# Kernel optimization log

Measured on AMD Instinct MI355X. Metric: run time of the kernel, lower is better.

## Reference

```python
import jax, jax.numpy as jnp
import numpy as np

LN_EPS = 1e-5

def _linear(x, W, b):
    # torch nn.Linear equivalent with W stored as [in, out]
    return jnp.einsum('bsd,de->bse', x, W) + b

def setup_inputs() -> dict:
    key = jax.random.key(0)
    ks = jax.random.split(key, 8)
    B, S, D = 4, 4096, 1024
    scale = 0.02
    inp = {
        'x': jax.random.normal(ks[0], (B, S, D), dtype=jnp.float32),
        'Wk': jax.random.normal(ks[1], (D, D), dtype=jnp.float32) * scale,
        'bk': jnp.zeros((D,), jnp.float32),
        'Wv': jax.random.normal(ks[2], (D, D), dtype=jnp.float32) * scale,
        'bv': jnp.zeros((D,), jnp.float32),
        'Wq': jax.random.normal(ks[3], (D, D), dtype=jnp.float32) * scale,
        'bq': jnp.zeros((D,), jnp.float32),
        'Wkp': jax.random.normal(ks[4], (D, D), dtype=jnp.float32) * scale,
        'bkp': jnp.zeros((D,), jnp.float32),
        'Wqp': jax.random.normal(ks[5], (D, D), dtype=jnp.float32) * scale,
        'bqp': jnp.zeros((D,), jnp.float32),
        'ln_g': jnp.ones((D,), jnp.float32),
        'ln_b': jnp.zeros((D,), jnp.float32),
        'Wo': jax.random.normal(ks[6], (D, D), dtype=jnp.float32) * scale,
        'bo': jnp.zeros((D,), jnp.float32),
        'idx': jax.random.permutation(ks[7], S)[:32].astype(jnp.int32),
        'chunk_size': 64,
    }
    return inp

def _ortho_loss(kc, ks_, idx):
    # sample rows, pairwise Re(conj(z_i) z_j) = cos_i cos_j + sin_i sin_j
    B, _, D = kc.shape
    n = idx.shape[0]
    cs = kc[:, idx, :]                                # [B, n, D]
    sn = ks_[:, idx, :]
    dot = cs[:, :, None, :] * cs[:, None, :, :] + sn[:, :, None, :] * sn[:, None, :, :]  # [B,n,n,D]
    mask = (~jnp.eye(n, dtype=bool))[None, :, :, None].astype(dot.dtype)
    denom = jnp.float32(n * (n - 1)) * D + 1e-6       # mask.sum() * dim + eps
    return jnp.sum(dot * dot * mask) / denom

def reference(x, Wk, bk, Wv, bv, Wq, bq, Wkp, bkp, Wqp, bqp, ln_g, ln_b, Wo, bo, idx, chunk_size):
    B, S, D = x.shape
    key = _linear(x, Wk, bk)
    value = _linear(x, Wv, bv)
    query = _linear(x, Wq, bq)
    key_phase = _linear(key, Wkp, bkp)
    query_phase = _linear(query, Wqp, bqp)
    kc, ksin = jnp.cos(key_phase), jnp.sin(key_phase)
    qc, qsin = jnp.cos(query_phase), jnp.sin(query_phase)
    ortho = _ortho_loss(kc, ksin, idx)
    br = value * kc
    bi = value * ksin
    pad = (-S) % chunk_size
    if pad > 0:
        pw = ((0, 0), (0, pad), (0, 0))
        br = jnp.pad(br, pw); bi = jnp.pad(bi, pw)
        qc = jnp.pad(qc, pw); qsin = jnp.pad(qsin, pw)
    P = S + pad
    nc = P // chunk_size
    shp = (B, nc, chunk_size, D)
    mem_r = jnp.cumsum(br.reshape(shp), axis=2)
    mem_i = jnp.cumsum(bi.reshape(shp), axis=2)
    retrieved = mem_r * qc.reshape(shp) + mem_i * qsin.reshape(shp)
    retrieved = retrieved.reshape(B, P, D)[:, :S]
    retrieved = retrieved / jnp.sqrt(jnp.float32(S))
    mu = jnp.mean(retrieved, axis=-1, keepdims=True)
    var = jnp.var(retrieved, axis=-1, keepdims=True)
    ln = (retrieved - mu) * jax.lax.rsqrt(var + LN_EPS) * ln_g + ln_b
    out = x + _linear(ln, Wo, bo)
    return out, ortho
```

## Files before the change

### kernel.cpp

```cpp
#include <hip/hip_runtime.h>
#include <math.h>

#define D_DIM 1024
#define S_DIM 4096
#define B_DIM 4
#define CHUNK 64
#define NC (S_DIM / CHUNK)
#define M_DIM (B_DIM * S_DIM)
#define MD ((size_t)M_DIM * D_DIM)

typedef __bf16 bf16_t;
typedef __attribute__((ext_vector_type(8))) __bf16 bf16x8;
typedef __attribute__((ext_vector_type(4))) __bf16 bf16x4;
typedef __attribute__((ext_vector_type(2))) __bf16 bf16x2;
typedef __attribute__((ext_vector_type(4))) float f32x4;

__device__ __forceinline__ void async_copy16(const void* g, void* lds) {
  __builtin_amdgcn_global_load_lds(
      (const __attribute__((address_space(1))) unsigned int*)g,
      (__attribute__((address_space(3))) unsigned int*)lds, 16, 0, 0);
}

#define SB __builtin_amdgcn_s_barrier()
#define PRIO1 __builtin_amdgcn_s_setprio(1)
#define PRIO0 __builtin_amdgcn_s_setprio(0)

template <int MODE>
__global__ __launch_bounds__(512, 2) void gemm256(const bf16_t* __restrict__ A,
                                                  const bf16_t* __restrict__ Bt,
                                                  const float* __restrict__ bias,
                                                  const float* __restrict__ res,
                                                  float* __restrict__ Cf,
                                                  bf16_t* __restrict__ Cb) {
  constexpr int K = D_DIM;
  constexpr int NB_N = (MODE == 0) ? 12 : 4;
  __shared__ bf16_t sm[65536];

  const int bid = blockIdx.x;
  const int xcd = bid & 7;
  const int slot = bid >> 3;
  const int bm = (xcd * 8 + slot / NB_N) * 256;
  const int bn = (slot % NB_N) * 256;

  const int tid = threadIdx.x;
  const int lane = tid & 63;
  const int wave = tid >> 6;
  const int wm = wave >> 2;
  const int wn = wave & 3;
  const int quad = lane >> 4;
  const int l15 = lane & 15;
  const int lane8 = lane * 8;
  const int bg = (wn & 1) * 4;

  const int c0 = tid, c1 = tid + 512;
#define ROWOF(c) ((((c) >> 7) & 7) * 16 + ((c) & 15))
#define KGOF(c) ((((c) >> 6) & 1) * 4 + (((c) >> 4) & 3))
  const bf16_t* gA0 = A + (size_t)(bm + ROWOF(c0)) * K + KGOF(c0) * 8;
  const bf16_t* gA1 = A + (size_t)(bm + ROWOF(c1)) * K + KGOF(c1) * 8;
  const bf16_t* gB0 = Bt + (size_t)(bn + ROWOF(c0)) * K + KGOF(c0) * 8;
  const bf16_t* gB1 = Bt + (size_t)(bn + ROWOF(c1)) * K + KGOF(c1) * 8;

  bf16_t* stA0 = sm + wave * 512;
  bf16_t* stB0 = sm + 16384 + wave * 512;
  bf16_t* stA1 = sm + 32768 + wave * 512;
  bf16_t* stB1 = sm + 49152 + wave * 512;
  const bf16_t* A0p = sm + wm * 8192 + lane8;
  const bf16_t* B0p = sm + 16384 + (wn >> 1) * 8192 + lane8;
  const bf16_t* A1p = sm + 32768 + wm * 8192 + lane8;
  const bf16_t* B1p = sm + 49152 + (wn >> 1) * 8192 + lane8;

#define STG(gp0, gp1, kofs, db, hx)                                        \
  do {                                                                     \
    async_copy16(gp0 + (size_t)(hx)*131072 + (kofs), (db) + (hx)*8192);    \
    async_copy16(gp1 + (size_t)(hx)*131072 + (kofs), (db) + (hx)*8192 + 4096); \
  } while (0)

  f32x4 acc[8][4];
#pragma unroll
  for (int i = 0; i < 8; i++)
#pragma unroll
    for (int j = 0; j < 4; j++) acc[i][j] = (f32x4){0.f, 0.f, 0.f, 0.f};

  bf16x8 af[4][2], bl[2][2], bh[2][2];

#define RDA(P, MS)                                                         \
  _Pragma("unroll") for (int m = 0; m < 4; ++m) {                          \
    af[m][0] = *(const bf16x8*)((P) + (((MS) + m) * 2 + 0) * 512);         \
    af[m][1] = *(const bf16x8*)((P) + (((MS) + m) * 2 + 1) * 512);         \
  }
#define RDB(P, DST, NS)                                                    \
  _Pragma("unroll") for (int n = 0; n < 2; ++n) {                          \
    DST[n][0] = *(const bf16x8*)((P) + (((NS) + n) * 2 + 0) * 512);        \
    DST[n][1] = *(const bf16x8*)((P) + (((NS) + n) * 2 + 1) * 512);        \
  }
#define MFQ(MB, NB, BB)                                                    \
  do {                                                                     \
    PRIO1;                                                                 \
    _Pragma("unroll") for (int m = 0; m < 4; ++m)                          \
        _Pragma("unroll") for (int n = 0; n < 2; ++n) {                    \
      acc[(MB) + m][(NB) + n] = __builtin_amdgcn_mfma_f32_16x16x32_bf16(   \
          af[m][0], BB[n][0], acc[(MB) + m][(NB) + n], 0, 0, 0);           \
      acc[(MB) + m][(NB) + n] = __builtin_amdgcn_mfma_f32_16x16x32_bf16(   \
          af[m][1], BB[n][1], acc[(MB) + m][(NB) + n], 0, 0, 0);           \
    }                                                                      \
    PRIO0;                                                                 \
  } while (0)

  STG(gB0, gB1, 0, stB0, 0);
  STG(gB0, gB1, 0, stB0, 1);
  STG(gA0, gA1, 0, stA0, 0);
  STG(gA0, gA1, 0, stA0, 1);
  STG(gB0, gB1, 64, stB1, 0);
  STG(gB0, gB1, 64, stB1, 1);
  asm volatile("s_waitcnt vmcnt(4)" ::: "memory");
  SB;

  for (int i = 0; i < 8; ++i) {
    const size_t kA1 = (size_t)(2 * i + 1) * 64;
    const size_t kN = (size_t)(2 * i + 2) * 64;
    const bool pf = (i < 7);

    RDA(A0p, 0);
    RDB(B0p, bl, bg);
    STG(gA0, gA1, kA1, stA1, 0);
    SB; MFQ(0, 0, bl); SB;

    RDB(B0p, bh, bg + 2);
    STG(gA0, gA1, kA1, stA1, 1);
    SB; MFQ(0, 2, bh); SB;

    RDA(A0p, 4);
    if (pf) STG(gB0, gB1, kN, stB0, 0);
    SB; MFQ(4, 2, bh); SB;

    if (pf) STG(gB0, gB1, kN, stB0, 1);
    SB; MFQ(4, 0, bl);
    if (pf) { asm volatile("s_waitcnt vmcnt(4)" ::: "memory"); }
    else    { asm volatile("s_waitcnt vmcnt(0)" ::: "memory"); }
    SB;

    RDA(A1p, 0);
    RDB(B1p, bl, bg);
    if (pf) STG(gA0, gA1, kN, stA0, 0);
    SB; MFQ(0, 0, bl); SB;

    RDB(B1p, bh, bg + 2);
    if (pf) STG(gA0, gA1, kN, stA0, 1);
    SB; MFQ(0, 2, bh); SB;

    RDA(A1p, 4);
    if (pf) STG(gB0, gB1, kN + 64, stB1, 0);
    SB; MFQ(4, 2, bh); SB;

    if (pf) STG(gB0, gB1, kN + 64, stB1, 1);
    SB; MFQ(4, 0, bl);
    if (pf) { asm volatile("s_waitcnt vmcnt(4)" ::: "memory"); }
    else    { asm volatile("s_waitcnt vmcnt(0)" ::: "memory"); }
    SB;
  }
  __builtin_amdgcn_sched_barrier(0);

  const int baserow = bm + wm * 128;
  const int basecol = bn + wn * 64 + l15;
  float bvv[4];
#pragma unroll
  for (int nf = 0; nf < 4; ++nf) bvv[nf] = bias[basecol + nf * 16];
#pragma unroll
  for (int mf = 0; mf < 8; ++mf) {
#pragma unroll
    for (int r = 0; r < 4; ++r) {
      const int m = baserow + mf * 16 + quad * 4 + r;
#pragma unroll
      for (int nf = 0; nf < 4; ++nf) {
        const int n = basecol + nf * 16;
        float v = acc[mf][nf][r] + bvv[nf];
        if (MODE == 2) {
          v += res[(size_t)m * D_DIM + n];
          Cf[(size_t)m * D_DIM + n] = v;
        } else {
          Cb[(size_t)(n >> 10) * MD + (size_t)m * D_DIM + (n & 1023)] =
              (bf16_t)v;
        }
      }
    }
  }
#undef ROWOF
#undef KGOF
#undef STG
#undef RDA
#undef RDB
#undef MFQ
}

template <int MODE>
__global__ __launch_bounds__(256) void gemm_mfma(const bf16_t* __restrict__ A,
                                                 const bf16_t* __restrict__ Bt,
                                                 const float* __restrict__ bias,
                                                 const float* __restrict__ res,
                                                 float* __restrict__ Cf,
                                                 bf16_t* __restrict__ Cb) {
  constexpr int K = D_DIM;
  constexpr int NB_N = (MODE == 0) ? 24 : 8;
  constexpr int NB_M = (MODE == 3) ? 16 : 128;
  __shared__ bf16_t sm[4 * 4096];

  const int bid = blockIdx.x;
  const int xcd = bid & 7;
  const int slot = bid >> 3;
  const int bm = (xcd * (NB_M / 8) + slot / NB_N) * 128;
  const int bn = (slot % NB_N) * 128;

  const int tid = threadIdx.x;
  const int lane = tid & 63;
  const int wave = tid >> 6;
  const int wm = wave & 1, wn = wave >> 1;
  const int quad = lane >> 4;
  const int l15 = lane & 15;

  bf16_t* As0 = sm;
  bf16_t* As1 = sm + 4096;
  bf16_t* Bs0 = sm + 8192;
  bf16_t* Bs1 = sm + 12288;

  const bf16_t* BtP = Bt;
  if (MODE == 3) BtP = Bt + (size_t)(bm >> 10) * D_DIM * D_DIM;

  f32x4 acc[4][4];
#pragma unroll
  for (int i = 0; i < 4; i++)
#pragma unroll
    for (int j = 0; j < 4; j++) acc[i][j] = (f32x4){0.f, 0.f, 0.f, 0.f};

  const int e0 = tid, e1 = tid + 256;
  const int wofs = wave * 512;
  const bf16_t* a0 = A + (size_t)(bm + (e0 >> 2)) * K + (e0 & 3) * 8;
  const bf16_t* a1 = A + (size_t)(bm + (e1 >> 2)) * K + (e1 & 3) * 8;
  const bf16_t* b0 = BtP + (size_t)(bn + (e0 >> 2)) * K + (e0 & 3) * 8;
  const bf16_t* b1 = BtP + (size_t)(bn + (e1 >> 2)) * K + (e1 & 3) * 8;

  for (int k0 = 0; k0 < K; k0 += 64) {
    async_copy16(a0 + k0, As0 + wofs);
    async_copy16(a1 + k0, As0 + 2048 + wofs);
    async_copy16(b0 + k0, Bs0 + wofs);
    async_copy16(b1 + k0, Bs0 + 2048 + wofs);
    async_copy16(a0 + k0 + 32, As1 + wofs);
    async_copy16(a1 + k0 + 32, As1 + 2048 + wofs);
    async_copy16(b0 + k0 + 32, Bs1 + wofs);
    async_copy16(b1 + k0 + 32, Bs1 + 2048 + wofs);
    __syncthreads();

#pragma unroll
    for (int h = 0; h < 2; h++) {
      const bf16_t* Ah = h ? As1 : As0;
      const bf16_t* Bh = h ? Bs1 : Bs0;
      bf16x8 af[4], bfr[4];
#pragma unroll
      for (int t = 0; t < 4; t++) {
        af[t] = *(const bf16x8*)(Ah + (size_t)(wm * 64 + t * 16 + l15) * 32 + quad * 8);
        bfr[t] = *(const bf16x8*)(Bh + (size_t)(wn * 64 + t * 16 + l15) * 32 + quad * 8);
      }
#pragma unroll
      for (int mt = 0; mt < 4; mt++)
#pragma unroll
        for (int nt = 0; nt < 4; nt++)
          acc[mt][nt] =
              __builtin_amdgcn_mfma_f32_16x16x32_bf16(af[mt], bfr[nt], acc[mt][nt], 0, 0, 0);
    }
    __syncthreads();
  }

  const int baserow = bm + wm * 64;
  const int basecol = bn + wn * 64 + l15;
#pragma unroll
  for (int mt = 0; mt < 4; mt++) {
#pragma unroll
    for (int nt = 0; nt < 4; nt++) {
      const int n = basecol + nt * 16;
      const float bv = (MODE == 3) ? 0.f : bias[n];
#pragma unroll
      for (int r = 0; r < 4; r++) {
        const int m = baserow + mt * 16 + quad * 4 + r;
        float v = acc[mt][nt][r] + bv;
        if (MODE == 2) {
          v += res[(size_t)m * D_DIM + n];
          Cf[(size_t)m * D_DIM + n] = v;
        } else if (MODE == 0) {
          Cb[(size_t)(bn >> 10) * MD + (size_t)m * D_DIM + (n & 1023)] = (bf16_t)v;
        } else {
          Cb[(size_t)(bm >> 10) * D_DIM * D_DIM + (size_t)(m & 1023) * D_DIM + n] =
              (bf16_t)v;
        }
      }
    }
  }
}

__global__ __launch_bounds__(256) void prep_all(
    const float* __restrict__ s0, const float* __restrict__ s1,
    const float* __restrict__ s2, const float* __restrict__ s3,
    bf16_t* __restrict__ d0, bf16_t* __restrict__ d1,
    bf16_t* __restrict__ d2, bf16_t* __restrict__ d3,
    const float* __restrict__ x, const float* __restrict__ Wk,
    const float* __restrict__ Wq, bf16_t* __restrict__ xb,
    bf16_t* __restrict__ wkb, bf16_t* __restrict__ wqb) {
  const int z = blockIdx.z;
  if (z < 4) {
    const float* srcs[4] = {s0, s1, s2, s3};
    bf16_t* dsts[4] = {d0, d1, d2, d3};
    const float* W = srcs[z];
    bf16_t* Wt = dsts[z];
    __shared__ float tile[32][33];
    const int bx = blockIdx.x * 32;
    const int by = blockIdx.y * 32;
    const int tx = threadIdx.x & 31, ty = threadIdx.x >> 5;
#pragma unroll
    for (int r = 0; r < 32; r += 8)
      tile[ty + r][tx] = W[(size_t)(by + ty + r) * D_DIM + bx + tx];
    __syncthreads();
#pragma unroll
    for (int r = 0; r < 32; r += 8)
      Wt[(size_t)(bx + ty + r) * D_DIM + by + tx] = (bf16_t)tile[tx][ty + r];
  } else {
    size_t i = ((size_t)(z - 4) * 1024 + blockIdx.y * 32 + blockIdx.x) * 256 +
               threadIdx.x;
    const float* src;
    bf16_t* dst;
    size_t off;
    if (i < 4194304) { src = x; dst = xb; off = i; }
    else if (i < 4456448) { src = Wk; dst = wkb; off = i - 4194304; }
    else { src = Wq; dst = wqb; off = i - 4456448; }
    const float4 v = ((const float4*)src)[off];
    bf16x4 o;
    o[0] = (bf16_t)v.x; o[1] = (bf16_t)v.y; o[2] = (bf16_t)v.z; o[3] = (bf16_t)v.w;
    ((bf16x4*)dst)[off] = o;
  }
}

__global__ __launch_bounds__(256) void fused_bias_k(
    const float* __restrict__ bv, const float* __restrict__ bk,
    const float* __restrict__ bkp, const float* __restrict__ bq,
    const float* __restrict__ bqp, const float* __restrict__ Wkp,
    const float* __restrict__ Wqp, float* __restrict__ fb) {
  const int n = blockIdx.x * 256 + threadIdx.x;
  const int t = n >> 10, c = n & 1023;
  if (t == 0) {
    fb[n] = bv[c];
    return;
  }
  const float* W = (t == 1) ? Wkp : Wqp;
  const float* b1 = (t == 1) ? bk : bq;
  const float* b2 = (t == 1) ? bkp : bqp;
  float s = b2[c];
#pragma unroll 8
  for (int k = 0; k < D_DIM; k++) s = fmaf(b1[k], W[(size_t)k * D_DIM + c], s);
  fb[n] = s;
}

__global__ __launch_bounds__(512) void scan_ln(const bf16_t* __restrict__ vb,
                                               const bf16_t* __restrict__ kp,
                                               const bf16_t* __restrict__ qp,
                                               const float* __restrict__ g,
                                               const float* __restrict__ bl,
                                               bf16_t* __restrict__ outb) {
  __shared__ bf16_t retl[32 * 1024];
  const int chunk = blockIdx.x;
  const int b = blockIdx.y;
  const int tid = threadIdx.x;
  const int lane = tid & 63, wave = tid >> 6;
  const int c = tid * 2;
  const size_t base = ((size_t)(b * S_DIM + chunk * CHUNK)) * D_DIM + c;
  float2 mr = {0.f, 0.f}, mi = {0.f, 0.f};
  const float inv = 0.015625f;

  for (int half = 0; half < 2; half++) {
    for (int s8 = 0; s8 < 32; s8++) {
      const int s = half * 32 + s8;
      const size_t off = base + (size_t)s * D_DIM;
      bf16x2 v2 = *(const bf16x2*)(vb + off);
      bf16x2 k2 = *(const bf16x2*)(kp + off);
      bf16x2 q2 = *(const bf16x2*)(qp + off);
      float sk, ck, sq, cq;
      __sincosf((float)k2[0], &sk, &ck);
      mr.x = fmaf((float)v2[0], ck, mr.x);
      mi.x = fmaf((float)v2[0], sk, mi.x);
      __sincosf((float)k2[1], &sk, &ck);
      mr.y = fmaf((float)v2[1], ck, mr.y);
      mi.y = fmaf((float)v2[1], sk, mi.y);
      bf16x2 r;
      __sincosf((float)q2[0], &sq, &cq);
      r[0] = (bf16_t)((mr.x * cq + mi.x * sq) * inv);
      __sincosf((float)q2[1], &sq, &cq);
      r[1] = (bf16_t)((mr.y * cq + mi.y * sq) * inv);
      *(bf16x2*)(retl + s8 * 1024 + c) = r;
    }
    __syncthreads();
#pragma unroll
    for (int j = 0; j < 4; j++) {
      const int r8 = wave * 4 + j;
      const int col0 = lane * 16;
      const bf16x8 va = *(const bf16x8*)(retl + r8 * 1024 + col0);
      const bf16x8 vb8 = *(const bf16x8*)(retl + r8 * 1024 + col0 + 8);
      float vf[16];
#pragma unroll
      for (int k = 0; k < 8; k++) { vf[k] = (float)va[k]; vf[8 + k] = (float)vb8[k]; }
      float s = 0.f, ss = 0.f;
#pragma unroll
      for (int k = 0; k < 16; k++) { s += vf[k]; ss += vf[k] * vf[k]; }
#pragma unroll
      for (int o = 32; o > 0; o >>= 1) {
        s += __shfl_down(s, o);
        ss += __shfl_down(ss, o);
      }
      s = __shfl(s, 0);
      ss = __shfl(ss, 0);
      const float mu = s * (1.f / D_DIM);
      const float var = ss * (1.f / D_DIM) - mu * mu;
      const float rs = 1.f / sqrtf(var + 1e-5f);
      const int m = b * S_DIM + chunk * CHUNK + half * 32 + r8;
      bf16x8 o1, o2;
#pragma unroll
      for (int q = 0; q < 4; q++) {
        const float4 gv = *(const float4*)(g + col0 + 4 * q);
        const float4 bv = *(const float4*)(bl + col0 + 4 * q);
        const int kbase = 4 * q;
        float r0 = (vf[kbase + 0] - mu) * rs * gv.x + bv.x;
        float r1 = (vf[kbase + 1] - mu) * rs * gv.y + bv.y;
        float r2 = (vf[kbase + 2] - mu) * rs * gv.z + bv.z;
        float r3 = (vf[kbase + 3] - mu) * rs * gv.w + bv.w;
        if (q < 2) {
          o1[kbase + 0] = (bf16_t)r0; o1[kbase + 1] = (bf16_t)r1;
          o1[kbase + 2] = (bf16_t)r2; o1[kbase + 3] = (bf16_t)r3;
        } else {
          o2[kbase - 8] = (bf16_t)r0; o2[kbase - 7] = (bf16_t)r1;
          o2[kbase - 6] = (bf16_t)r2; o2[kbase - 5] = (bf16_t)r3;
        }
      }
      *(bf16x8*)(outb + (size_t)m * D_DIM + col0) = o1;
      *(bf16x8*)(outb + (size_t)m * D_DIM + col0 + 8) = o2;
    }
    __syncthreads();
  }
}

__global__ __launch_bounds__(256) void ortho_partial(const bf16_t* __restrict__ kp,
                                                     const int* __restrict__ idx,
                                                     float* __restrict__ partial) {
  const int i = blockIdx.x;
  const int b = blockIdx.y;
  const int ri = idx[i];
  const bf16x4 ab = *(const bf16x4*)(kp + ((size_t)b * S_DIM + ri) * D_DIM + threadIdx.x * 4);
  float a0 = (float)ab[0], a1 = (float)ab[1], a2 = (float)ab[2], a3 = (float)ab[3];
  float sum = 0.f;
  for (int j = 0; j < 32; j++) {
    if (j == i) continue;
    const int rj = idx[j];
    const bf16x4 cb = *(const bf16x4*)(kp + ((size_t)b * S_DIM + rj) * D_DIM + threadIdx.x * 4);
    float d0 = __cosf(a0 - (float)cb[0]);
    float d1 = __cosf(a1 - (float)cb[1]);
    float d2 = __cosf(a2 - (float)cb[2]);
    float d3 = __cosf(a3 - (float)cb[3]);
    sum += d0 * d0 + d1 * d1 + d2 * d2 + d3 * d3;
  }
#pragma unroll
  for (int o = 32; o > 0; o >>= 1) sum += __shfl_down(sum, o);
  __shared__ float red[4];
  if ((threadIdx.x & 63) == 0) red[threadIdx.x >> 6] = sum;
  __syncthreads();
  if (threadIdx.x == 0) partial[b * 32 + i] = red[0] + red[1] + red[2] + red[3];
}

__global__ void ortho_final(const float* __restrict__ partial, float* __restrict__ outp) {
  if (threadIdx.x == 0) {
    double s = 0.0;
    for (int t = 0; t < 128; t++) s += (double)partial[t];
    const double denom = (double)(32 * 31) * 1024.0 + 1e-6;
    outp[0] = (float)(s / denom);
  }
}

extern "C" void kernel_launch(void* const* d_in, const int* in_sizes, int n_in,
                              void* d_out, int out_size, void* d_ws, size_t ws_size,
                              hipStream_t stream) {
  const float* x = (const float*)d_in[0];
  const float* Wk = (const float*)d_in[1];
  const float* bk = (const float*)d_in[2];
  const float* Wv = (const float*)d_in[3];
  const float* bv = (const float*)d_in[4];
  const float* Wq = (const float*)d_in[5];
  const float* bq = (const float*)d_in[6];
  const float* Wkp = (const float*)d_in[7];
  const float* bkp = (const float*)d_in[8];
  const float* Wqp = (const float*)d_in[9];
  const float* bqp = (const float*)d_in[10];
  const float* ln_g = (const float*)d_in[11];
  const float* ln_b = (const float*)d_in[12];
  const float* Wo = (const float*)d_in[13];
  const float* bo = (const float*)d_in[14];
  const int* idx = (const int*)d_in[15];

  float* out = (float*)d_out;
  float* ortho_out = out + MD;

  char* ws = (char*)d_ws;
  const size_t MB = 1024 * 1024;
  bf16_t* QKVT = (bf16_t*)(ws + 0 * MB);
  bf16_t* WoT = (bf16_t*)(ws + 6 * MB);
  bf16_t* WkpT2 = (bf16_t*)(ws + 8 * MB);
  float* fbias = (float*)(ws + 12 * MB);
  float* partial = (float*)(ws + 12 * MB + 16 * 1024);
  bf16_t* Wkqb = (bf16_t*)(ws + 13 * MB);
  bf16_t* xb = (bf16_t*)(ws + 32 * MB);
  bf16_t* mega_out = (bf16_t*)(ws + 64 * MB);
  bf16_t* kp_b = mega_out + MD;
  bf16_t* qp_b = mega_out + 2 * MD;
  bf16_t* lnb = (bf16_t*)(ws + 32 * MB);

  prep_all<<<dim3(32, 32, 22), 256, 0, stream>>>(
      Wv, Wkp, Wqp, Wo, QKVT, WkpT2, WkpT2 + (size_t)D_DIM * D_DIM, WoT,
      x, Wk, Wq, xb, Wkqb, Wkqb + (size_t)D_DIM * D_DIM);
  gemm_mfma<3><<<128, 256, 0, stream>>>(WkpT2, Wkqb, nullptr, nullptr, nullptr,
                                        QKVT + (size_t)D_DIM * D_DIM);
  fused_bias_k<<<12, 256, 0, stream>>>(bv, bk, bkp, bq, bqp, Wkp, Wqp, fbias);

  gemm256<0><<<768, 512, 0, stream>>>(xb, QKVT, fbias, nullptr, nullptr,
                                      mega_out);
  ortho_partial<<<dim3(32, B_DIM), 256, 0, stream>>>(kp_b, idx, partial);
  scan_ln<<<dim3(NC, B_DIM), 512, 0, stream>>>(mega_out, kp_b, qp_b, ln_g, ln_b,
                                               lnb);
  gemm256<2><<<256, 512, 0, stream>>>(lnb, WoT, bo, x, out, nullptr);
  ortho_final<<<1, 64, 0, stream>>>(partial, ortho_out);
}
```

Measured before the change: 438.2 us.

## Deepen GEMM load pipelining with split A fragments and reorder tile rasterization

The GEMM main loop now keeps two A-fragment register sets, one for the low and one for the high M half. All B fragments for a sub-step are read up front, and async global-to-LDS copies for A are issued one stage earlier, with the vmcnt waits raised to match. Block-to-tile mapping changes so that consecutive slots within an XCD walk M first rather than N, which changes which tiles share L2. The goal is to hide LDS and global latency behind MFMA work. The cost is extra VGPR pressure under the 2-blocks-per-CU launch bound, and a different cache reuse pattern.

```diff
diff --git a/kernel.cpp b/kernel.cpp
--- a/kernel.cpp
+++ b/kernel.cpp
@@ -33,14 +33,13 @@
                                                   float* __restrict__ Cf,
                                                   bf16_t* __restrict__ Cb) {
   constexpr int K = D_DIM;
-  constexpr int NB_N = (MODE == 0) ? 12 : 4;
   __shared__ bf16_t sm[65536];
 
   const int bid = blockIdx.x;
   const int xcd = bid & 7;
   const int slot = bid >> 3;
-  const int bm = (xcd * 8 + slot / NB_N) * 256;
-  const int bn = (slot % NB_N) * 256;
+  const int bm = (xcd * 8 + (slot & 7)) * 256;
+  const int bn = (slot >> 3) * 256;
 
   const int tid = threadIdx.x;
   const int lane = tid & 63;
@@ -81,27 +80,27 @@
 #pragma unroll
     for (int j = 0; j < 4; j++) acc[i][j] = (f32x4){0.f, 0.f, 0.f, 0.f};
 
-  bf16x8 af[4][2], bl[2][2], bh[2][2];
-
-#define RDA(P, MS)                                                         \
+  bf16x8 afL[4][2], afH[4][2], bl[2][2], bh[2][2];
+
+#define RDA(P, MS, AA)                                                     \
   _Pragma("unroll") for (int m = 0; m < 4; ++m) {                          \
-    af[m][0] = *(const bf16x8*)((P) + (((MS) + m) * 2 + 0) * 512);         \
-    af[m][1] = *(const bf16x8*)((P) + (((MS) + m) * 2 + 1) * 512);         \
+    AA[m][0] = *(const bf16x8*)((P) + (((MS) + m) * 2 + 0) * 512);         \
+    AA[m][1] = *(const bf16x8*)((P) + (((MS) + m) * 2 + 1) * 512);         \
   }
 #define RDB(P, DST, NS)                                                    \
   _Pragma("unroll") for (int n = 0; n < 2; ++n) {                          \
     DST[n][0] = *(const bf16x8*)((P) + (((NS) + n) * 2 + 0) * 512);        \
     DST[n][1] = *(const bf16x8*)((P) + (((NS) + n) * 2 + 1) * 512);        \
   }
-#define MFQ(MB, NB, BB)                                                    \
+#define MFQ(MB, NB, BB, AA)                                                \
   do {                                                                     \
     PRIO1;                                                                 \
     _Pragma("unroll") for (int m = 0; m < 4; ++m)                          \
         _Pragma("unroll") for (int n = 0; n < 2; ++n) {                    \
       acc[(MB) + m][(NB) + n] = __builtin_amdgcn_mfma_f32_16x16x32_bf16(   \
-          af[m][0], BB[n][0], acc[(MB) + m][(NB) + n], 0, 0, 0);           \
+          AA[m][0], BB[n][0], acc[(MB) + m][(NB) + n], 0, 0, 0);           \
       acc[(MB) + m][(NB) + n] = __builtin_amdgcn_mfma_f32_16x16x32_bf16(   \
-          af[m][1], BB[n][1], acc[(MB) + m][(NB) + n], 0, 0, 0);           \
+          AA[m][1], BB[n][1], acc[(MB) + m][(NB) + n], 0, 0, 0);           \
     }                                                                      \
     PRIO0;                                                                 \
   } while (0)
@@ -112,7 +111,8 @@
   STG(gA0, gA1, 0, stA0, 1);
   STG(gB0, gB1, 64, stB1, 0);
   STG(gB0, gB1, 64, stB1, 1);
-  asm volatile("s_waitcnt vmcnt(4)" ::: "memory");
+  STG(gA0, gA1, 64, stA1, 0);
+  asm volatile("s_waitcnt vmcnt(6)" ::: "memory");
   SB;
 
   for (int i = 0; i < 8; ++i) {
@@ -120,41 +120,39 @@
     const size_t kN = (size_t)(2 * i + 2) * 64;
     const bool pf = (i < 7);
 
-    RDA(A0p, 0);
+    STG(gA0, gA1, kA1, stA1, 1);
+    RDA(A0p, 0, afL);
     RDB(B0p, bl, bg);
-    STG(gA0, gA1, kA1, stA1, 0);
-    SB; MFQ(0, 0, bl); SB;
-
     RDB(B0p, bh, bg + 2);
-    STG(gA0, gA1, kA1, stA1, 1);
-    SB; MFQ(0, 2, bh); SB;
-
-    RDA(A0p, 4);
+    SB; MFQ(0, 0, bl, afL); SB;
+
+    RDA(A0p, 4, afH);
+    SB; MFQ(0, 2, bh, afL); SB;
+
     if (pf) STG(gB0, gB1, kN, stB0, 0);
-    SB; MFQ(4, 2, bh); SB;
-
-    if (pf) STG(gB0, gB1, kN, stB0, 1);
-    SB; MFQ(4, 0, bl);
-    if (pf) { asm volatile("s_waitcnt vmcnt(4)" ::: "memory"); }
+    SB; MFQ(4, 2, bh, afH); SB;
+
+    if (pf) { STG(gB0, gB1, kN, stB0, 1); STG(gA0, gA1, kN, stA0, 0); }
+    SB; MFQ(4, 0, bl, afH);
+    if (pf) { asm volatile("s_waitcnt vmcnt(6)" ::: "memory"); }
     else    { asm volatile("s_waitcnt vmcnt(0)" ::: "memory"); }
     SB;
 
-    RDA(A1p, 0);
+    if (pf) STG(gA0, gA1, kN, stA0, 1);
+    RDA(A1p, 0, afL);
     RDB(B1p, bl, bg);
-    if (pf) STG(gA0, gA1, kN, stA0, 0);
-    SB; MFQ(0, 0, bl); SB;
-
     RDB(B1p, bh, bg + 2);
-    if (pf) STG(gA0, gA1, kN, stA0, 1);
-    SB; MFQ(0, 2, bh); SB;
-
-    RDA(A1p, 4);
+    SB; MFQ(0, 0, bl, afL); SB;
+
+    RDA(A1p, 4, afH);
+    SB; MFQ(0, 2, bh, afL); SB;
+
     if (pf) STG(gB0, gB1, kN + 64, stB1, 0);
-    SB; MFQ(4, 2, bh); SB;
-
-    if (pf) STG(gB0, gB1, kN + 64, stB1, 1);
-    SB; MFQ(4, 0, bl);
-    if (pf) { asm volatile("s_waitcnt vmcnt(4)" ::: "memory"); }
+    SB; MFQ(4, 2, bh, afH); SB;
+
+    if (pf) { STG(gB0, gB1, kN + 64, stB1, 1); STG(gA0, gA1, kN + 64, stA1, 0); }
+    SB; MFQ(4, 0, bl, afH);
+    if (pf) { asm volatile("s_waitcnt vmcnt(6)" ::: "memory"); }
     else    { asm volatile("s_waitcnt vmcnt(0)" ::: "memory"); }
     SB;
   }
```

After: 447.9 us. +2.2%, slower.
